# Performance work log

Hardware: AMD Instinct MI355X
Metric: run time of the kernel (lower is better)

## Reference

```python
import jax, jax.numpy as jnp
import numpy as np

N_USERS = 100000
N_ITEMS = 50000
N_ENTITIES = 150000
N_EDGES = 2000000
NNZ = 1000000
CHANNEL = 64
N_HOPS = 2
TEMPERATURE = 0.2
PDIST_EPS = 1e-6   # torch.nn.PairwiseDistance default eps (added to the diff)
NORM_EPS = 1e-12   # F.normalize default eps


def setup_inputs() -> dict:
    key = jax.random.key(0)
    ks = jax.random.split(key, 8)
    return {
        "user_emb": jax.random.normal(ks[0], (N_USERS, CHANNEL), dtype=jnp.float32),
        "entity_emb": jax.random.normal(ks[1], (N_ENTITIES, CHANNEL), dtype=jnp.float32),
        "weight": jax.random.normal(ks[2], (20, CHANNEL), dtype=jnp.float32),
        "edge_index": jax.random.randint(ks[3], (2, N_EDGES), 0, N_ENTITIES, dtype=jnp.int64) if jax.config.jax_enable_x64 else jax.random.randint(ks[3], (2, N_EDGES), 0, N_ENTITIES, dtype=jnp.int32),
        "edge_type": jax.random.randint(ks[4], (N_EDGES,), 0, 20, dtype=jnp.int32),
        "inter_user": jax.random.randint(ks[5], (NNZ,), 0, N_USERS, dtype=jnp.int32),
        "inter_item": jax.random.randint(ks[6], (NNZ,), 0, N_ITEMS, dtype=jnp.int32),
        "inter_vals": jax.random.uniform(ks[7], (NNZ,), dtype=jnp.float32),
    }


def _l2_normalize(x):
    # F.normalize(x, p=2, dim=1): x / max(||x||, eps)
    n = jnp.sqrt(jnp.sum(x * x, axis=-1, keepdims=True))
    return x / jnp.maximum(n, NORM_EPS)


def _aggregate(entity_emb, head, tail, inter_user, inter_item, inter_vals):
    n_entities = entity_emb.shape[0]
    # scatter_mean over KG edges: mean of tail embeddings per head entity
    neigh = entity_emb[tail]                                   # [E, C]
    summed = jax.ops.segment_sum(neigh, head, num_segments=n_entities)
    cnt = jax.ops.segment_sum(jnp.ones((head.shape[0],), entity_emb.dtype), head,
                              num_segments=n_entities)
    entity_agg = summed / jnp.maximum(cnt, 1.0)[:, None]       # [n_entities, C]

    items = entity_agg[:N_ITEMS]                               # [n_items, C]
    g_items = items[inter_item]                                # [nnz, C]
    # user_mean = interact_map @ entity_agg[:n_items]  (sparse mm via segment_sum)
    user_mean = jax.ops.segment_sum(inter_vals[:, None] * g_items, inter_user,
                                    num_segments=N_USERS)      # [n_users, C]
    # pairwise L2 distance per interaction edge
    diff = g_items - user_mean[inter_user] + PDIST_EPS
    score = jnp.sqrt(jnp.sum(diff * diff, axis=-1)) / TEMPERATURE   # [nnz]
    # sparse softmax over each user row
    row_max = jax.ops.segment_max(score, inter_user, num_segments=N_USERS)
    e = jnp.exp(score - row_max[inter_user])
    denom = jax.ops.segment_sum(e, inter_user, num_segments=N_USERS)
    soft = e / denom[inter_user]                               # [nnz]
    # user_agg = soft_score_mat @ entity_agg[:n_items]
    user_agg = jax.ops.segment_sum(soft[:, None] * g_items, inter_user,
                                   num_segments=N_USERS)       # [n_users, C]
    return user_agg, entity_agg


def reference(user_emb, entity_emb, weight, edge_index, edge_type,
              inter_user, inter_item, inter_vals):
    # GraphConv.forward with mess_dropout=False, node_dropout=False (deterministic)
    head, tail = edge_index[0], edge_index[1]
    user_res, entity_res = user_emb, entity_emb
    u, ent = user_emb, entity_emb
    for _ in range(N_HOPS):
        u, ent = _aggregate(ent, head, tail, inter_user, inter_item, inter_vals)
        ent = _l2_normalize(ent)
        u = _l2_normalize(u)
        entity_res = entity_res + ent
        user_res = user_res + u
    return user_res, entity_res
```

## Files before the change

### kernel.cpp

```cpp
#include <hip/hip_runtime.h>

#define N_USERS   100000
#define N_ITEMS   50000
#define N_ENT     150000
#define N_EDGES   2000000
#define NNZ       1000000
#define CH        64

#define CB_SHIFT  9
#define CB_SIZE   512
#define NB_E      ((N_ENT   + CB_SIZE - 1) >> CB_SHIFT)
#define NB_U      ((N_USERS + CB_SIZE - 1) >> CB_SHIFT)
#define A_CHUNK   4096
#define UCACHE    32
#define ECAP      8192
#define UCAP      6144

#define NBLK_CONV  ((N_ENT * 16 + 255) / 256)
#define NBLK_BS_E  ((N_EDGES + A_CHUNK - 1) / A_CHUNK)
#define NBLK_BS_U  ((NNZ + A_CHUNK - 1) / A_CHUNK)
#define GB_G8      ((N_ENT + 31) / 32)
#define GB_USER    (N_USERS / 4)
#define G2U1_NG    1563

typedef __fp16 h2v __attribute__((ext_vector_type(2)));

__device__ __forceinline__ h2v h2z() { h2v z = {(__fp16)0.f, (__fp16)0.f}; return z; }
__device__ __forceinline__ h2v pk(float a, float b) { return __builtin_amdgcn_cvt_pkrtz(a, b); }
__device__ __forceinline__ unsigned int h2u(h2v h) { return __builtin_bit_cast(unsigned int, h); }
__device__ __forceinline__ h2v u2h(unsigned int u) { return __builtin_bit_cast(h2v, u); }
__device__ __forceinline__ float fdot2f(h2v a, h2v b, float c) {
    return __builtin_amdgcn_fdot2(a, b, c, false);
}

template<int CTRL>
__device__ __forceinline__ float dpp_mov(float x) {
    return __builtin_bit_cast(float, __builtin_amdgcn_update_dpp(
        0, __builtin_bit_cast(int, x), CTRL, 0xF, 0xF, true));
}
template<int CTRL>
__device__ __forceinline__ unsigned dpp_mov_u(unsigned x) {
    return (unsigned)__builtin_amdgcn_update_dpp(0, (int)x, CTRL, 0xF, 0xF, true);
}
__device__ __forceinline__ float red8(float x) {
    x += dpp_mov<0xB1>(x);
    x += dpp_mov<0x4E>(x);
    x += dpp_mov<0x141>(x);
    return x;
}
__device__ __forceinline__ h2v grpadd8(h2v a) {
    return a + u2h(dpp_mov_u<0x128>(h2u(a)));
}


__device__ __forceinline__ void binscat_ent_f(const int* __restrict__ head,
                                              const int* __restrict__ tail,
                                              unsigned int* __restrict__ cur,
                                              unsigned int* __restrict__ binned,
                                              unsigned int* h, unsigned int* bb, int bid) {
    int lo = bid * A_CHUNK;
    int hi = min(lo + A_CHUNK, N_EDGES);
    for (int i = threadIdx.x; i < NB_E; i += blockDim.x) h[i] = 0;
    __syncthreads();
    for (int e = lo + threadIdx.x; e < hi; e += blockDim.x)
        atomicAdd(&h[head[e] >> CB_SHIFT], 1u);
    __syncthreads();
    for (int i = threadIdx.x; i < NB_E; i += blockDim.x) {
        unsigned int c = h[i];
        bb[i] = c ? ((unsigned int)i * ECAP + atomicAdd(&cur[i], c)) : 0u;
        h[i] = 0;
    }
    __syncthreads();
    for (int e = lo + threadIdx.x; e < hi; e += blockDim.x) {
        int hd = head[e];
        int b = hd >> CB_SHIFT;
        unsigned int r = atomicAdd(&h[b], 1u);
        unsigned int local = (unsigned int)hd & (CB_SIZE - 1);
        binned[bb[b] + r] = (local << 18) | (unsigned int)tail[e];
    }
}

__device__ __forceinline__ void binscat_user_f(const int* __restrict__ iu,
                                               const int* __restrict__ ii,
                                               const float* __restrict__ iv,
                                               unsigned int* __restrict__ cur,
                                               unsigned int* __restrict__ binned,
                                               float* __restrict__ binnedv,
                                               unsigned int* h, unsigned int* bb, int bid) {
    int lo = bid * A_CHUNK;
    int hi = min(lo + A_CHUNK, NNZ);
    for (int i = threadIdx.x; i < NB_U; i += blockDim.x) h[i] = 0;
    __syncthreads();
    for (int e = lo + threadIdx.x; e < hi; e += blockDim.x)
        atomicAdd(&h[iu[e] >> CB_SHIFT], 1u);
    __syncthreads();
    for (int i = threadIdx.x; i < NB_U; i += blockDim.x) {
        unsigned int c = h[i];
        bb[i] = c ? ((unsigned int)i * UCAP + atomicAdd(&cur[i], c)) : 0u;
        h[i] = 0;
    }
    __syncthreads();
    for (int e = lo + threadIdx.x; e < hi; e += blockDim.x) {
        int u = iu[e];
        int b = u >> CB_SHIFT;
        unsigned int r = atomicAdd(&h[b], 1u);
        unsigned int slot = bb[b] + r;
        unsigned int local = (unsigned int)u & (CB_SIZE - 1);
        binned[slot] = (local << 16) | (unsigned int)ii[e];
        binnedv[slot] = iv[e];
    }
}

__global__ void build_d1(const int* __restrict__ head, const int* __restrict__ tail,
                         const int* __restrict__ iu, const int* __restrict__ ii,
                         const float* __restrict__ iv,
                         const float* __restrict__ entity_emb, uint2* __restrict__ E0,
                         unsigned int* __restrict__ curE, unsigned int* __restrict__ binnedE,
                         unsigned int* __restrict__ curU, unsigned int* __restrict__ binnedU,
                         float* __restrict__ binnedUV) {
    __shared__ unsigned int h[NB_E];
    __shared__ unsigned int bb[NB_E];
    int bid = blockIdx.x;
    if (bid < NBLK_BS_E) {
        binscat_ent_f(head, tail, curE, binnedE, h, bb, bid);
    } else if (bid < NBLK_BS_E + NBLK_BS_U) {
        binscat_user_f(iu, ii, iv, curU, binnedU, binnedUV, h, bb, bid - NBLK_BS_E);
    } else {
        int i = (bid - NBLK_BS_E - NBLK_BS_U) * 256 + threadIdx.x;
        if (i < N_ENT * 16) {
            float4 a = ((const float4*)entity_emb)[i];
            E0[i] = make_uint2(h2u(pk(a.x, a.y)), h2u(pk(a.z, a.w)));
        }
    }
}

__device__ __forceinline__ void csort_ent_f(const unsigned int* __restrict__ cnt,
                                            const unsigned int* __restrict__ binned,
                                            int* __restrict__ col,
                                            uint2* __restrict__ erow,
                                            unsigned int* h, unsigned int* ex,
                                            unsigned int* pairs, int b) {
    unsigned int s0 = (unsigned int)b * ECAP;
    unsigned int n  = min(cnt[b], (unsigned int)ECAP);
    unsigned int s1 = s0 + n;
    int t = threadIdx.x;
    h[2 * t] = 0; h[2 * t + 1] = 0;
    __syncthreads();
    for (unsigned int j = s0 + t; j < s1; j += 256)
        atomicAdd(&h[binned[j] >> 18], 1u);
    __syncthreads();
    unsigned int a0 = h[2 * t], a1 = h[2 * t + 1];
    pairs[t] = a0 + a1;
    __syncthreads();
    for (int off = 1; off < 256; off <<= 1) {
        unsigned int u = 0;
        if (t >= off) u = pairs[t - off];
        __syncthreads();
        if (t >= off) pairs[t] += u;
        __syncthreads();
    }
    unsigned int pe = pairs[t] - (a0 + a1);
    ex[2 * t] = pe;
    ex[2 * t + 1] = pe + a0;
    __syncthreads();
    int keybase = b << CB_SHIFT;
    if (keybase + 2 * t < N_ENT)     erow[keybase + 2 * t]     = make_uint2(s0 + ex[2 * t], a0);
    if (keybase + 2 * t + 1 < N_ENT) erow[keybase + 2 * t + 1] = make_uint2(s0 + ex[2 * t + 1], a1);
    __syncthreads();
    h[2 * t] = 0; h[2 * t + 1] = 0;
    __syncthreads();
    for (unsigned int j = s0 + t; j < s1; j += 256) {
        unsigned int p = binned[j];
        unsigned int local = p >> 18;
        unsigned int r = atomicAdd(&h[local], 1u);
        col[s0 + ex[local] + r] = (int)(p & 0x3FFFFu);
    }
}

__device__ __forceinline__ void csort_user_f(const unsigned int* __restrict__ cnt,
                                             const unsigned int* __restrict__ binned,
                                             const float* __restrict__ binnedv,
                                             int2* __restrict__ upair,
                                             uint2* __restrict__ urow,
                                             unsigned int* h, unsigned int* ex,
                                             unsigned int* pairs, int b) {
    unsigned int s0 = (unsigned int)b * UCAP;
    unsigned int n  = min(cnt[b], (unsigned int)UCAP);
    unsigned int s1 = s0 + n;
    int t = threadIdx.x;
    h[2 * t] = 0; h[2 * t + 1] = 0;
    __syncthreads();
    for (unsigned int j = s0 + t; j < s1; j += 256)
        atomicAdd(&h[binned[j] >> 16], 1u);
    __syncthreads();
    unsigned int a0 = h[2 * t], a1 = h[2 * t + 1];
    pairs[t] = a0 + a1;
    __syncthreads();
    for (int off = 1; off < 256; off <<= 1) {
        unsigned int u = 0;
        if (t >= off) u = pairs[t - off];
        __syncthreads();
        if (t >= off) pairs[t] += u;
        __syncthreads();
    }
    unsigned int pe = pairs[t] - (a0 + a1);
    ex[2 * t] = pe;
    ex[2 * t + 1] = pe + a0;
    __syncthreads();
    int keybase = b << CB_SHIFT;
    if (keybase + 2 * t < N_USERS)     urow[keybase + 2 * t]     = make_uint2(s0 + ex[2 * t], a0);
    if (keybase + 2 * t + 1 < N_USERS) urow[keybase + 2 * t + 1] = make_uint2(s0 + ex[2 * t + 1], a1);
    __syncthreads();
    h[2 * t] = 0; h[2 * t + 1] = 0;
    __syncthreads();
    for (unsigned int j = s0 + t; j < s1; j += 256) {
        unsigned int p = binned[j];
        float v = binnedv[j];
        unsigned int local = p >> 16;
        unsigned int r = atomicAdd(&h[local], 1u);
        upair[s0 + ex[local] + r] = make_int2((int)(p & 0xFFFFu), __float_as_int(v));
    }
}

__global__ void build_d2(const unsigned int* __restrict__ curE,
                         const unsigned int* __restrict__ binnedE,
                         int* __restrict__ col, uint2* __restrict__ erow) {
    __shared__ unsigned int h[CB_SIZE];
    __shared__ unsigned int ex[CB_SIZE];
    __shared__ unsigned int pairs[256];
    csort_ent_f(curE, binnedE, col, erow, h, ex, pairs, blockIdx.x);
}


__device__ __forceinline__ void gather_fin_row8(int row, int t, bool valid,
        const uint4* __restrict__ entb, const uint2* __restrict__ erow,
        const int* __restrict__ col,
        uint4* __restrict__ ent_out, uint4* __restrict__ items_out,
        const float* __restrict__ base_ent, const uint4* __restrict__ v1tab,
        float* __restrict__ out_ent, int mode) {
    unsigned int s0 = 0, deg = 0;
    if (valid) { uint2 rs = erow[row]; s0 = rs.x; deg = rs.y; }
    unsigned int s1 = s0 + deg;

    h2v a0 = h2z(), a1 = h2z(), a2 = h2z(), a3 = h2z();
    unsigned int j = s0;
    for (; j + 3 < s1; j += 4) {
        int c0 = col[j], c1 = col[j + 1], c2 = col[j + 2], c3 = col[j + 3];
        uint4 x0 = entb[(size_t)c0 * 8 + t];
        uint4 x1 = entb[(size_t)c1 * 8 + t];
        uint4 x2 = entb[(size_t)c2 * 8 + t];
        uint4 x3 = entb[(size_t)c3 * 8 + t];
        a0 += (u2h(x0.x) + u2h(x1.x)) + (u2h(x2.x) + u2h(x3.x));
        a1 += (u2h(x0.y) + u2h(x1.y)) + (u2h(x2.y) + u2h(x3.y));
        a2 += (u2h(x0.z) + u2h(x1.z)) + (u2h(x2.z) + u2h(x3.z));
        a3 += (u2h(x0.w) + u2h(x1.w)) + (u2h(x2.w) + u2h(x3.w));
    }
    for (; j < s1; ++j) {
        uint4 x = entb[(size_t)col[j] * 8 + t];
        a0 += u2h(x.x); a1 += u2h(x.y); a2 += u2h(x.z); a3 += u2h(x.w);
    }
    float inv = 1.0f / fmaxf((float)deg, 1.0f);
    float m0 = (float)a0[0] * inv, m1 = (float)a0[1] * inv;
    float m2 = (float)a1[0] * inv, m3 = (float)a1[1] * inv;
    float m4 = (float)a2[0] * inv, m5 = (float)a2[1] * inv;
    float m6 = (float)a3[0] * inv, m7 = (float)a3[1] * inv;

    float sq = m0*m0 + m1*m1 + m2*m2 + m3*m3 + m4*m4 + m5*m5 + m6*m6 + m7*m7;
    sq = red8(sq);
    float invn = 1.0f / fmaxf(sqrtf(sq), 1e-12f);

    if (!valid) return;
    size_t o = (size_t)row * 8 + t;
    if (row < N_ITEMS)
        items_out[o] = make_uint4(h2u(pk(m0, m1)), h2u(pk(m2, m3)),
                                  h2u(pk(m4, m5)), h2u(pk(m6, m7)));
    if (mode == 0) {
        ent_out[o] = make_uint4(h2u(pk(m0*invn, m1*invn)), h2u(pk(m2*invn, m3*invn)),
                                h2u(pk(m4*invn, m5*invn)), h2u(pk(m6*invn, m7*invn)));
    } else {
        size_t fo = (size_t)row * 16 + 2 * t;
        float4 c0 = ((const float4*)base_ent)[fo];
        float4 c1 = ((const float4*)base_ent)[fo + 1];
        uint4 v1 = v1tab[o];
        h2v p0 = u2h(v1.x), p1 = u2h(v1.y), p2 = u2h(v1.z), p3 = u2h(v1.w);
        ((float4*)out_ent)[fo]     = make_float4(c0.x + (float)p0[0] + m0*invn,
                                                 c0.y + (float)p0[1] + m1*invn,
                                                 c0.z + (float)p1[0] + m2*invn,
                                                 c0.w + (float)p1[1] + m3*invn);
        ((float4*)out_ent)[fo + 1] = make_float4(c1.x + (float)p2[0] + m4*invn,
                                                 c1.y + (float)p2[1] + m5*invn,
                                                 c1.z + (float)p3[0] + m6*invn,
                                                 c1.w + (float)p3[1] + m7*invn);
    }
}

template<int NS>
__device__ __forceinline__ void user_fast_path(
        unsigned int s0, unsigned int deg, int grp, int t,
        const uint4* __restrict__ itemsb, const int2* __restrict__ up,
        float& l, h2v& ac0, h2v& ac1, h2v& ac2, h2v& ac3) {
    const float SC = 5.0f * 1.44269504f;
    uint4 r[NS];
    float vw[NS];
    #pragma unroll
    for (int k = 0; k < NS; ++k) {
        unsigned int slot = (unsigned int)grp + 8u * k;
        if (slot < deg) {
            int2 p = up[s0 + slot];
            r[k] = itemsb[(size_t)p.x * 8 + t];
            vw[k] = __int_as_float(p.y);
        } else {
            r[k] = make_uint4(0u, 0u, 0u, 0u);
            vw[k] = 0.0f;
        }
    }
    h2v um0 = h2z(), um1 = h2z(), um2 = h2z(), um3 = h2z();
    #pragma unroll
    for (int k = 0; k < NS; ++k) {
        h2v v2 = pk(vw[k], vw[k]);
        um0 += v2 * u2h(r[k].x); um1 += v2 * u2h(r[k].y);
        um2 += v2 * u2h(r[k].z); um3 += v2 * u2h(r[k].w);
    }
    um0 = grpadd8(um0); um1 = grpadd8(um1); um2 = grpadd8(um2); um3 = grpadd8(um3);
    #pragma unroll
    for (int m = 16; m <= 32; m <<= 1) {
        um0 += u2h(__shfl_xor(h2u(um0), m, 64));
        um1 += u2h(__shfl_xor(h2u(um1), m, 64));
        um2 += u2h(__shfl_xor(h2u(um2), m, 64));
        um3 += u2h(__shfl_xor(h2u(um3), m, 64));
    }
    float scv[NS];
    float mloc = -1e30f;
    #pragma unroll
    for (int k = 0; k < NS; ++k) {
        unsigned int slot = (unsigned int)grp + 8u * k;
        h2v d0 = u2h(r[k].x) - um0, d1 = u2h(r[k].y) - um1;
        h2v d2 = u2h(r[k].z) - um2, d3 = u2h(r[k].w) - um3;
        float sq = fdot2f(d3, d3, fdot2f(d2, d2, fdot2f(d1, d1, fdot2f(d0, d0, 0.0f))));
        sq = red8(sq);
        float sc = sqrtf(sq) * SC;
        scv[k] = (slot < deg) ? sc : -1e30f;
        mloc = fmaxf(mloc, scv[k]);
    }
    mloc = fmaxf(mloc, dpp_mov<0x128>(mloc));
    float M = fmaxf(mloc, __shfl_xor(mloc, 16, 64));
    M = fmaxf(M, __shfl_xor(M, 32, 64));
    #pragma unroll
    for (int k = 0; k < NS; ++k) {
        float e = exp2f(scv[k] - M);
        l += e;
        h2v e2 = pk(e, e);
        ac0 += e2 * u2h(r[k].x); ac1 += e2 * u2h(r[k].y);
        ac2 += e2 * u2h(r[k].z); ac3 += e2 * u2h(r[k].w);
    }
}

__device__ __forceinline__ void fused_user_row(int row, int lane, uint4 (*cw)[8],
        const uint4* __restrict__ itemsb, const uint2* __restrict__ urow,
        const int2* __restrict__ up, const float* __restrict__ base_user,
        float* __restrict__ out_user) {
    int grp = lane >> 3;
    int t   = lane & 7;
    uint2 rs = urow[row];
    unsigned int s0 = rs.x;
    unsigned int deg = rs.y;
    unsigned int s1 = s0 + deg;

    const float SC = 5.0f * 1.44269504f;
    float l = 0.0f;
    h2v ac0 = h2z(), ac1 = h2z(), ac2 = h2z(), ac3 = h2z();

    if (__builtin_expect(deg <= 16, 1)) {
        user_fast_path<2>(s0, deg, grp, t, itemsb, up, l, ac0, ac1, ac2, ac3);
    } else if (deg <= UCACHE) {
        user_fast_path<4>(s0, deg, grp, t, itemsb, up, l, ac0, ac1, ac2, ac3);
    } else {
        h2v um0 = h2z(), um1 = h2z(), um2 = h2z(), um3 = h2z();
        for (unsigned int j = s0 + grp; j < s1; j += 8) {
            int2 p = up[j];
            uint4 r = itemsb[(size_t)p.x * 8 + t];
            int slot = (int)(j - s0);
            if (slot < UCACHE) cw[slot][t] = r;
            float v = __int_as_float(p.y);
            h2v v2 = pk(v, v);
            um0 += v2 * u2h(r.x); um1 += v2 * u2h(r.y);
            um2 += v2 * u2h(r.z); um3 += v2 * u2h(r.w);
        }
        um0 = grpadd8(um0); um1 = grpadd8(um1); um2 = grpadd8(um2); um3 = grpadd8(um3);
        #pragma unroll
        for (int m = 16; m <= 32; m <<= 1) {
            um0 += u2h(__shfl_xor(h2u(um0), m, 64));
            um1 += u2h(__shfl_xor(h2u(um1), m, 64));
            um2 += u2h(__shfl_xor(h2u(um2), m, 64));
            um3 += u2h(__shfl_xor(h2u(um3), m, 64));
        }
        float m_run = -1e30f;
        for (unsigned int j = s0 + grp; j < s1; j += 8) {
            int slot = (int)(j - s0);
            uint4 r = (slot < UCACHE) ? cw[slot][t]
                                      : itemsb[(size_t)up[j].x * 8 + t];
            h2v d0 = u2h(r.x) - um0, d1 = u2h(r.y) - um1;
            h2v d2 = u2h(r.z) - um2, d3 = u2h(r.w) - um3;
            float sq = fdot2f(d3, d3, fdot2f(d2, d2, fdot2f(d1, d1, fdot2f(d0, d0, 0.0f))));
            sq = red8(sq);
            float sc = sqrtf(sq) * SC;
            if (sc > m_run) {
                float s = exp2f(m_run - sc);
                l *= s;
                h2v s2 = pk(s, s);
                ac0 *= s2; ac1 *= s2; ac2 *= s2; ac3 *= s2;
                m_run = sc;
            }
            float e = exp2f(sc - m_run);
            l += e;
            h2v e2 = pk(e, e);
            ac0 += e2 * u2h(r.x); ac1 += e2 * u2h(r.y);
            ac2 += e2 * u2h(r.z); ac3 += e2 * u2h(r.w);
        }
        float mx = fmaxf(m_run, dpp_mov<0x128>(m_run));
        float M = fmaxf(mx, __shfl_xor(mx, 16, 64));
        M = fmaxf(M, __shfl_xor(M, 32, 64));
        float wgt = (l > 0.0f) ? exp2f(m_run - M) : 0.0f;
        l *= wgt;
        h2v w2 = pk(wgt, wgt);
        ac0 *= w2; ac1 *= w2; ac2 *= w2; ac3 *= w2;
    }

    l = l + dpp_mov<0x128>(l);
    ac0 = grpadd8(ac0); ac1 = grpadd8(ac1); ac2 = grpadd8(ac2); ac3 = grpadd8(ac3);
    #pragma unroll
    for (int m = 16; m <= 32; m <<= 1) {
        l   += __shfl_xor(l, m, 64);
        ac0 += u2h(__shfl_xor(h2u(ac0), m, 64));
        ac1 += u2h(__shfl_xor(h2u(ac1), m, 64));
        ac2 += u2h(__shfl_xor(h2u(ac2), m, 64));
        ac3 += u2h(__shfl_xor(h2u(ac3), m, 64));
    }
    float invl = (l > 0.0f) ? (1.0f / l) : 0.0f;
    float u0 = (float)ac0[0] * invl, u1 = (float)ac0[1] * invl;
    float u2 = (float)ac1[0] * invl, u3 = (float)ac1[1] * invl;
    float u4 = (float)ac2[0] * invl, u5 = (float)ac2[1] * invl;
    float u6 = (float)ac3[0] * invl, u7 = (float)ac3[1] * invl;

    float sq2 = u0*u0 + u1*u1 + u2*u2 + u3*u3 + u4*u4 + u5*u5 + u6*u6 + u7*u7;
    sq2 = red8(sq2);
    float inv = 1.0f / fmaxf(sqrtf(sq2), 1e-12f);
    if (grp == 0) {
        size_t fo = (size_t)row * 16 + 2 * t;
        float4 c0 = ((const float4*)base_user)[fo];
        float4 c1 = ((const float4*)base_user)[fo + 1];
        ((float4*)out_user)[fo]     = make_float4(c0.x + u0*inv, c0.y + u1*inv,
                                                  c0.z + u2*inv, c0.w + u3*inv);
        ((float4*)out_user)[fo + 1] = make_float4(c1.x + u4*inv, c1.y + u5*inv,
                                                  c1.z + u6*inv, c1.w + u7*inv);
    }
}


__global__ void gf1_p4u_k(const uint4* __restrict__ E0,
                          const uint2* __restrict__ erow,
                          const int* __restrict__ col,
                          uint4* __restrict__ E1, uint4* __restrict__ itemsA,
                          const unsigned int* __restrict__ curU,
                          const unsigned int* __restrict__ binnedU,
                          const float* __restrict__ binnedUV,
                          int2* __restrict__ upair, uint2* __restrict__ urow) {
    __shared__ unsigned int h[CB_SIZE];
    __shared__ unsigned int ex[CB_SIZE];
    __shared__ unsigned int pairs[256];
    int bid = blockIdx.x;
    if (bid < NB_U) {
        csort_user_f(curU, binnedU, binnedUV, upair, urow, h, ex, pairs, bid);
    } else {
        int lane = threadIdx.x & 63;
        int row = (bid - NB_U) * 32 + (threadIdx.x >> 6) * 8 + (lane >> 3);
        gather_fin_row8(row, lane & 7, row < N_ENT, E0, erow, col, E1, itemsA,
                        nullptr, nullptr, nullptr, 0);
    }
}

__global__ void g2_u1_k(const uint4* __restrict__ entb,
                        const uint2* __restrict__ erow,
                        const int* __restrict__ col,
                        uint4* __restrict__ items_out,
                        const float* __restrict__ entity_emb,
                        float* __restrict__ out_ent,
                        const uint4* __restrict__ itemsb1,
                        const uint2* __restrict__ urow,
                        const int2* __restrict__ up,
                        const float* __restrict__ base_user,
                        float* __restrict__ out_user) {
    __shared__ uint4 cache[4][UCACHE][8];
    int bid = blockIdx.x;
    int g = bid / 19, r = bid - g * 19;
    int w    = threadIdx.x >> 6;
    int lane = threadIdx.x & 63;
    if (r < 3) {
        int gb = g * 3 + r;
        int row = gb * 32 + w * 8 + (lane >> 3);
        gather_fin_row8(row, lane & 7, row < N_ENT, entb, erow, col,
                        nullptr, items_out, entity_emb, entb, out_ent, 1);
    } else {
        int idx = g * 16 + (r - 3);
        int row = idx * 4 + w;
        if (row < N_USERS)
            fused_user_row(row, lane, cache[w], itemsb1, urow, up,
                           base_user, out_user);
    }
}

__global__ void fused_user_k(const uint4* __restrict__ itemsb,
                             const uint2* __restrict__ urow,
                             const int2* __restrict__ up,
                             const float* __restrict__ base_user,
                             float* __restrict__ out_user) {
    __shared__ uint4 cache[4][UCACHE][8];
    int wave = (blockIdx.x * blockDim.x + threadIdx.x) >> 6;
    int w    = threadIdx.x >> 6;
    int lane = threadIdx.x & 63;
    if (wave >= N_USERS) return;
    fused_user_row(wave, lane, cache[w], itemsb, urow, up, base_user, out_user);
}

extern "C" void kernel_launch(void* const* d_in, const int* in_sizes, int n_in,
                              void* d_out, int out_size, void* d_ws, size_t ws_size,
                              hipStream_t stream) {
    const float* user_emb   = (const float*)d_in[0];
    const float* entity_emb = (const float*)d_in[1];
    const int*   edge_index = (const int*)d_in[3];
    const int*   iu = (const int*)d_in[5];
    const int*   ii = (const int*)d_in[6];
    const float* iv = (const float*)d_in[7];

    float* out_user = (float*)d_out;
    float* out_ent  = out_user + (size_t)N_USERS * CH;

    uint4* E0     = (uint4*)d_ws;
    uint4* E1     = E0 + (size_t)N_ENT * 8;
    uint4* itemsA = E1 + (size_t)N_ENT * 8;
    uint4* itemsB = itemsA + (size_t)N_ITEMS * 8;
    int2*  upair  = (int2*)(itemsB + (size_t)N_ITEMS * 8);
    int*   col    = (int*)(upair + (size_t)NB_U * UCAP);
    uint2* erow   = (uint2*)(col + (size_t)NB_E * ECAP);
    uint2* urow   = erow + N_ENT;
    unsigned int* curE = (unsigned int*)(urow + N_USERS);
    unsigned int* curU = curE + NB_E;

    unsigned int* binnedE  = (unsigned int*)E1;
    unsigned int* binnedU  = (unsigned int*)out_user;
    float*        binnedUV = (float*)(binnedU + (size_t)NB_U * UCAP);

    const int* head = edge_index;
    const int* tail = edge_index + N_EDGES;

    (void)hipMemsetAsync(curE, 0, (size_t)(NB_E + NB_U) * 4, stream);
    build_d1<<<NBLK_BS_E + NBLK_BS_U + NBLK_CONV, 256, 0, stream>>>(
        head, tail, iu, ii, iv, entity_emb, (uint2*)E0,
        curE, binnedE, curU, binnedU, binnedUV);
    build_d2<<<NB_E, 256, 0, stream>>>(curE, binnedE, col, erow);

    gf1_p4u_k<<<NB_U + GB_G8, 256, 0, stream>>>(E0, erow, col, E1, itemsA,
                                                curU, binnedU, binnedUV,
                                                upair, urow);

    g2_u1_k<<<G2U1_NG * 19, 256, 0, stream>>>(E1, erow, col, itemsB,
                                              entity_emb, out_ent,
                                              itemsA, urow, upair,
                                              user_emb, out_user);

    fused_user_k<<<GB_USER, 256, 0, stream>>>(itemsB, urow, upair,
                                              out_user, out_user);
}
```

Measured before the change: 399.5 us.

## Split hop-2 gather into item/non-item parts and overlap with user passes

The second-hop entity gather is split so the item rows (needed by the second user pass) run together with the first user pass, while the remaining non-item entity rows run alongside the second user pass. This drops the standalone user kernel and evens out work across the last two launches. The change also vectorises the binning loads to int4/float4 and rewrites the per-bin counting sort to use 512 threads with one key per thread. The 4-wide loads assume the chunk bounds are multiples of 4, which holds for these sizes.

```diff
diff --git a/kernel.cpp b/kernel.cpp
--- a/kernel.cpp
+++ b/kernel.cpp
@@ -20,8 +20,10 @@
 #define NBLK_BS_E  ((N_EDGES + A_CHUNK - 1) / A_CHUNK)
 #define NBLK_BS_U  ((NNZ + A_CHUNK - 1) / A_CHUNK)
 #define GB_G8      ((N_ENT + 31) / 32)
-#define GB_USER    (N_USERS / 4)
-#define G2U1_NG    1563
+#define GB_GI      ((N_ITEMS + 31) / 32)
+#define GB_GN      ((N_ENT - N_ITEMS) / 32)
+#define D4A_NG     1563
+#define D4B_NG     3125
 
 typedef __fp16 h2v __attribute__((ext_vector_type(2)));
 
@@ -60,10 +62,18 @@
                                               unsigned int* h, unsigned int* bb, int bid) {
     int lo = bid * A_CHUNK;
     int hi = min(lo + A_CHUNK, N_EDGES);
+    const int4* head4 = (const int4*)head;
+    const int4* tail4 = (const int4*)tail;
+    int lo4 = lo >> 2, hi4 = hi >> 2;
     for (int i = threadIdx.x; i < NB_E; i += blockDim.x) h[i] = 0;
     __syncthreads();
-    for (int e = lo + threadIdx.x; e < hi; e += blockDim.x)
-        atomicAdd(&h[head[e] >> CB_SHIFT], 1u);
+    for (int e4 = lo4 + threadIdx.x; e4 < hi4; e4 += blockDim.x) {
+        int4 hd = head4[e4];
+        atomicAdd(&h[hd.x >> CB_SHIFT], 1u);
+        atomicAdd(&h[hd.y >> CB_SHIFT], 1u);
+        atomicAdd(&h[hd.z >> CB_SHIFT], 1u);
+        atomicAdd(&h[hd.w >> CB_SHIFT], 1u);
+    }
     __syncthreads();
     for (int i = threadIdx.x; i < NB_E; i += blockDim.x) {
         unsigned int c = h[i];
@@ -71,12 +81,18 @@
         h[i] = 0;
     }
     __syncthreads();
-    for (int e = lo + threadIdx.x; e < hi; e += blockDim.x) {
-        int hd = head[e];
-        int b = hd >> CB_SHIFT;
-        unsigned int r = atomicAdd(&h[b], 1u);
-        unsigned int local = (unsigned int)hd & (CB_SIZE - 1);
-        binned[bb[b] + r] = (local << 18) | (unsigned int)tail[e];
+    for (int e4 = lo4 + threadIdx.x; e4 < hi4; e4 += blockDim.x) {
+        int4 hd = head4[e4];
+        int4 tl = tail4[e4];
+        int hds[4] = {hd.x, hd.y, hd.z, hd.w};
+        int tls[4] = {tl.x, tl.y, tl.z, tl.w};
+        #pragma unroll
+        for (int k = 0; k < 4; ++k) {
+            int b = hds[k] >> CB_SHIFT;
+            unsigned int r = atomicAdd(&h[b], 1u);
+            unsigned int local = (unsigned int)hds[k] & (CB_SIZE - 1);
+            binned[bb[b] + r] = (local << 18) | (unsigned int)tls[k];
+        }
     }
 }
 
@@ -89,10 +105,19 @@
                                                unsigned int* h, unsigned int* bb, int bid) {
     int lo = bid * A_CHUNK;
     int hi = min(lo + A_CHUNK, NNZ);
+    const int4*   iu4 = (const int4*)iu;
+    const int4*   ii4 = (const int4*)ii;
+    const float4* iv4 = (const float4*)iv;
+    int lo4 = lo >> 2, hi4 = hi >> 2;
     for (int i = threadIdx.x; i < NB_U; i += blockDim.x) h[i] = 0;
     __syncthreads();
-    for (int e = lo + threadIdx.x; e < hi; e += blockDim.x)
-        atomicAdd(&h[iu[e] >> CB_SHIFT], 1u);
+    for (int e4 = lo4 + threadIdx.x; e4 < hi4; e4 += blockDim.x) {
+        int4 u = iu4[e4];
+        atomicAdd(&h[u.x >> CB_SHIFT], 1u);
+        atomicAdd(&h[u.y >> CB_SHIFT], 1u);
+        atomicAdd(&h[u.z >> CB_SHIFT], 1u);
+        atomicAdd(&h[u.w >> CB_SHIFT], 1u);
+    }
     __syncthreads();
     for (int i = threadIdx.x; i < NB_U; i += blockDim.x) {
         unsigned int c = h[i];
@@ -100,14 +125,22 @@
         h[i] = 0;
     }
     __syncthreads();
-    for (int e = lo + threadIdx.x; e < hi; e += blockDim.x) {
-        int u = iu[e];
-        int b = u >> CB_SHIFT;
-        unsigned int r = atomicAdd(&h[b], 1u);
-        unsigned int slot = bb[b] + r;
-        unsigned int local = (unsigned int)u & (CB_SIZE - 1);
-        binned[slot] = (local << 16) | (unsigned int)ii[e];
-        binnedv[slot] = iv[e];
+    for (int e4 = lo4 + threadIdx.x; e4 < hi4; e4 += blockDim.x) {
+        int4   u = iu4[e4];
+        int4   it = ii4[e4];
+        float4 v = iv4[e4];
+        int us[4] = {u.x, u.y, u.z, u.w};
+        int is[4] = {it.x, it.y, it.z, it.w};
+        float vs[4] = {v.x, v.y, v.z, v.w};
+        #pragma unroll
+        for (int k = 0; k < 4; ++k) {
+            int b = us[k] >> CB_SHIFT;
+            unsigned int r = atomicAdd(&h[b], 1u);
+            unsigned int slot = bb[b] + r;
+            unsigned int local = (unsigned int)us[k] & (CB_SIZE - 1);
+            binned[slot] = (local << 16) | (unsigned int)is[k];
+            binnedv[slot] = vs[k];
+        }
     }
 }
 
@@ -134,46 +167,42 @@
     }
 }
 
-__device__ __forceinline__ void csort_ent_f(const unsigned int* __restrict__ cnt,
-                                            const unsigned int* __restrict__ binned,
-                                            int* __restrict__ col,
-                                            uint2* __restrict__ erow,
-                                            unsigned int* h, unsigned int* ex,
-                                            unsigned int* pairs, int b) {
+__global__ __launch_bounds__(512) void build_d2(const unsigned int* __restrict__ curE,
+                                                const unsigned int* __restrict__ binnedE,
+                                                int* __restrict__ col, uint2* __restrict__ erow) {
+    __shared__ unsigned int s[CB_SIZE];
+    __shared__ unsigned int hh[CB_SIZE];
+    int b = blockIdx.x;
+    int t = threadIdx.x;
     unsigned int s0 = (unsigned int)b * ECAP;
-    unsigned int n  = min(cnt[b], (unsigned int)ECAP);
+    unsigned int n  = min(curE[b], (unsigned int)ECAP);
     unsigned int s1 = s0 + n;
-    int t = threadIdx.x;
-    h[2 * t] = 0; h[2 * t + 1] = 0;
-    __syncthreads();
-    for (unsigned int j = s0 + t; j < s1; j += 256)
-        atomicAdd(&h[binned[j] >> 18], 1u);
-    __syncthreads();
-    unsigned int a0 = h[2 * t], a1 = h[2 * t + 1];
-    pairs[t] = a0 + a1;
-    __syncthreads();
-    for (int off = 1; off < 256; off <<= 1) {
+    hh[t] = 0;
+    __syncthreads();
+    for (unsigned int j = s0 + t; j < s1; j += 512)
+        atomicAdd(&hh[binnedE[j] >> 18], 1u);
+    __syncthreads();
+    unsigned int cnt = hh[t];
+    s[t] = cnt;
+    __syncthreads();
+    for (int off = 1; off < 512; off <<= 1) {
         unsigned int u = 0;
-        if (t >= off) u = pairs[t - off];
+        if (t >= off) u = s[t - off];
         __syncthreads();
-        if (t >= off) pairs[t] += u;
+        if (t >= off) s[t] += u;
         __syncthreads();
     }
-    unsigned int pe = pairs[t] - (a0 + a1);
-    ex[2 * t] = pe;
-    ex[2 * t + 1] = pe + a0;
-    __syncthreads();
-    int keybase = b << CB_SHIFT;
-    if (keybase + 2 * t < N_ENT)     erow[keybase + 2 * t]     = make_uint2(s0 + ex[2 * t], a0);
-    if (keybase + 2 * t + 1 < N_ENT) erow[keybase + 2 * t + 1] = make_uint2(s0 + ex[2 * t + 1], a1);
-    __syncthreads();
-    h[2 * t] = 0; h[2 * t + 1] = 0;
-    __syncthreads();
-    for (unsigned int j = s0 + t; j < s1; j += 256) {
-        unsigned int p = binned[j];
+    unsigned int ex = s[t] - cnt;
+    int key = (b << CB_SHIFT) + t;
+    if (key < N_ENT) erow[key] = make_uint2(s0 + ex, cnt);
+    s[t] = ex;
+    hh[t] = 0;
+    __syncthreads();
+    for (unsigned int j = s0 + t; j < s1; j += 512) {
+        unsigned int p = binnedE[j];
         unsigned int local = p >> 18;
-        unsigned int r = atomicAdd(&h[local], 1u);
-        col[s0 + ex[local] + r] = (int)(p & 0x3FFFFu);
+        unsigned int r = atomicAdd(&hh[local], 1u);
+        col[s0 + s[local] + r] = (int)(p & 0x3FFFFu);
     }
 }
 
@@ -220,15 +249,6 @@
         unsigned int r = atomicAdd(&h[local], 1u);
         upair[s0 + ex[local] + r] = make_int2((int)(p & 0xFFFFu), __float_as_int(v));
     }
-}
-
-__global__ void build_d2(const unsigned int* __restrict__ curE,
-                         const unsigned int* __restrict__ binnedE,
-                         int* __restrict__ col, uint2* __restrict__ erow) {
-    __shared__ unsigned int h[CB_SIZE];
-    __shared__ unsigned int ex[CB_SIZE];
-    __shared__ unsigned int pairs[256];
-    csort_ent_f(curE, binnedE, col, erow, h, ex, pairs, blockIdx.x);
 }
 
 
@@ -479,29 +499,28 @@
     }
 }
 
-__global__ void g2_u1_k(const uint4* __restrict__ entb,
-                        const uint2* __restrict__ erow,
-                        const int* __restrict__ col,
-                        uint4* __restrict__ items_out,
-                        const float* __restrict__ entity_emb,
-                        float* __restrict__ out_ent,
-                        const uint4* __restrict__ itemsb1,
-                        const uint2* __restrict__ urow,
-                        const int2* __restrict__ up,
-                        const float* __restrict__ base_user,
-                        float* __restrict__ out_user) {
+__global__ void g2i_u1_k(const uint4* __restrict__ entb,
+                         const uint2* __restrict__ erow,
+                         const int* __restrict__ col,
+                         uint4* __restrict__ items_out,
+                         const float* __restrict__ entity_emb,
+                         float* __restrict__ out_ent,
+                         const uint4* __restrict__ itemsb1,
+                         const uint2* __restrict__ urow,
+                         const int2* __restrict__ up,
+                         const float* __restrict__ base_user,
+                         float* __restrict__ out_user) {
     __shared__ uint4 cache[4][UCACHE][8];
     int bid = blockIdx.x;
-    int g = bid / 19, r = bid - g * 19;
+    int g = bid / 17, r = bid - g * 17;
     int w    = threadIdx.x >> 6;
     int lane = threadIdx.x & 63;
-    if (r < 3) {
-        int gb = g * 3 + r;
-        int row = gb * 32 + w * 8 + (lane >> 3);
-        gather_fin_row8(row, lane & 7, row < N_ENT, entb, erow, col,
+    if (r == 0) {
+        int row = g * 32 + w * 8 + (lane >> 3);
+        gather_fin_row8(row, lane & 7, row < N_ITEMS, entb, erow, col,
                         nullptr, items_out, entity_emb, entb, out_ent, 1);
     } else {
-        int idx = g * 16 + (r - 3);
+        int idx = g * 16 + (r - 1);
         int row = idx * 4 + w;
         if (row < N_USERS)
             fused_user_row(row, lane, cache[w], itemsb1, urow, up,
@@ -509,17 +528,30 @@
     }
 }
 
-__global__ void fused_user_k(const uint4* __restrict__ itemsb,
-                             const uint2* __restrict__ urow,
-                             const int2* __restrict__ up,
-                             const float* __restrict__ base_user,
-                             float* __restrict__ out_user) {
+__global__ void g2n_u2_k(const uint4* __restrict__ entb,
+                         const uint2* __restrict__ erow,
+                         const int* __restrict__ col,
+                         const float* __restrict__ entity_emb,
+                         float* __restrict__ out_ent,
+                         const uint4* __restrict__ itemsb2,
+                         const uint2* __restrict__ urow,
+                         const int2* __restrict__ up,
+                         float* __restrict__ out_user) {
     __shared__ uint4 cache[4][UCACHE][8];
-    int wave = (blockIdx.x * blockDim.x + threadIdx.x) >> 6;
+    int bid = blockIdx.x;
+    int g = bid / 9, r = bid - g * 9;
     int w    = threadIdx.x >> 6;
     int lane = threadIdx.x & 63;
-    if (wave >= N_USERS) return;
-    fused_user_row(wave, lane, cache[w], itemsb, urow, up, base_user, out_user);
+    if (r == 0) {
+        int row = N_ITEMS + g * 32 + w * 8 + (lane >> 3);
+        gather_fin_row8(row, lane & 7, row < N_ENT, entb, erow, col,
+                        nullptr, nullptr, entity_emb, entb, out_ent, 1);
+    } else {
+        int idx = g * 8 + (r - 1);
+        int row = idx * 4 + w;
+        fused_user_row(row, lane, cache[w], itemsb2, urow, up,
+                       out_user, out_user);
+    }
 }
 
 extern "C" void kernel_launch(void* const* d_in, const int* in_sizes, int n_in,
@@ -557,17 +589,19 @@
     build_d1<<<NBLK_BS_E + NBLK_BS_U + NBLK_CONV, 256, 0, stream>>>(
         head, tail, iu, ii, iv, entity_emb, (uint2*)E0,
         curE, binnedE, curU, binnedU, binnedUV);
-    build_d2<<<NB_E, 256, 0, stream>>>(curE, binnedE, col, erow);
+    build_d2<<<NB_E, 512, 0, stream>>>(curE, binnedE, col, erow);
 
     gf1_p4u_k<<<NB_U + GB_G8, 256, 0, stream>>>(E0, erow, col, E1, itemsA,
                                                 curU, binnedU, binnedUV,
                                                 upair, urow);
 
-    g2_u1_k<<<G2U1_NG * 19, 256, 0, stream>>>(E1, erow, col, itemsB,
+    g2i_u1_k<<<D4A_NG * 17, 256, 0, stream>>>(E1, erow, col, itemsB,
                                               entity_emb, out_ent,
                                               itemsA, urow, upair,
                                               user_emb, out_user);
 
-    fused_user_k<<<GB_USER, 256, 0, stream>>>(itemsB, urow, upair,
-                                              out_user, out_user);
-}
+    g2n_u2_k<<<D4B_NG * 9, 256, 0, stream>>>(E1, erow, col,
+                                             entity_emb, out_ent,
+                                             itemsB, urow, upair,
+                                             out_user);
+}
```

After: 371.2 us. 7.1% less time.
